# Kernel optimization log

Hardware: AMD Instinct MI355X
Metric: run time of the kernel (lower is better)

## Reference

```python
import jax, jax.numpy as jnp
import numpy as np

B, D, H = 32768, 256, 8
DH = D // H
SCALE = 1.0 / float(np.sqrt(DH))
# neighbor indices: for query node i, context = the other 3 nodes (in order)
NEIGH = np.array([[1, 2, 3], [0, 2, 3], [0, 1, 3], [0, 1, 2]], dtype=np.int32)


def setup_inputs() -> dict:
    key = jax.random.key(0)
    ks = jax.random.split(key, 6)
    s = 0.02
    mk = lambda k: jax.random.normal(k, (D, D), jnp.float32) * s
    return {
        "tokens": jax.random.normal(ks[0], (B, 4, D), jnp.float32),
        "Wq": mk(ks[1]),
        "Wk": mk(ks[2]),
        "Wv": mk(ks[3]),
        "Wr": mk(ks[4]),
        "Wo": mk(ks[5]),
        "ln_g": jnp.ones((D,), jnp.float32),
        "ln_b": jnp.zeros((D,), jnp.float32),
    }


def reference(tokens, Wq, Wk, Wv, Wr, Wo, ln_g, ln_b):
    # tokens: [B,4,D]. All 4 modality queries share one GCA block (share_gca=True),
    # so we batch the 4-node complete-graph message passing into one pass.
    neigh = jnp.asarray(NEIGH)
    ctx = tokens[:, neigh]                    # [B,4,3,D]
    Q = tokens @ Wq.T                         # [B,4,D]
    K = ctx @ Wk.T                            # [B,4,3,D]
    V = ctx @ Wv.T
    R = ctx @ Wr.T
    V_eff = jax.nn.sigmoid(R) * V             # gated values
    Qh = Q.reshape(B, 4, H, DH)
    Kh = K.reshape(B, 4, 3, H, DH)
    Vh = V_eff.reshape(B, 4, 3, H, DH)
    scores = jnp.einsum('bihd,bilhd->bihl', Qh, Kh) * SCALE   # [B,4,H,3]
    attn = jax.nn.softmax(scores, axis=-1)    # dropout = identity (eval mode)
    out = jnp.einsum('bihl,bilhd->bihd', attn, Vh).reshape(B, 4, D)
    out = out @ Wo.T
    y = tokens + out                          # residual
    mu = y.mean(-1, keepdims=True)
    var = y.var(-1, keepdims=True)
    y = (y - mu) / jnp.sqrt(var + 1e-5) * ln_g + ln_b   # LayerNorm
    # attn: [B,4,H,3] -> per-query attn maps (attn[:, i] == attn for modality-i query, [B,H,1,3] squeezed)
    return y, attn
```

## Files before the change

### kernel.cpp

```cpp
#include <hip/hip_runtime.h>
#include <stdint.h>


#define D_DIM   256
#define H_NUM   8
#define DH      32
#define RT      64
#define NTHR    1024
#define ROWS_TOT 131072
#define Y_SZ    33554432
#define SCALE_F 0.17677669529663687f
#define W_ELEMS 65536
#define WS_NEED (5 * W_ELEMS * 2)

#define SX_LD   264
#define SQK_LD  776
#define KOFF    256
#define VOFF    512
#define SY_LD   260

typedef __attribute__((ext_vector_type(8))) short bf16x8;
typedef __attribute__((ext_vector_type(4))) float f32x4;

__device__ __forceinline__ float b2f(uint16_t s) {
    union { uint32_t u; float f; } c; c.u = ((uint32_t)s) << 16; return c.f;
}
__device__ __forceinline__ uint16_t f2b(float f) {
    union { float f; uint32_t u; } c; c.f = f;
    return (uint16_t)((c.u + 0x7fffu + ((c.u >> 16) & 1u)) >> 16);
}
__device__ __forceinline__ bf16x8 cvt8(const float* p) {
    const float4 a = *(const float4*)p;
    const float4 b = *(const float4*)(p + 4);
    bf16x8 r;
    r[0] = (short)f2b(a.x); r[1] = (short)f2b(a.y);
    r[2] = (short)f2b(a.z); r[3] = (short)f2b(a.w);
    r[4] = (short)f2b(b.x); r[5] = (short)f2b(b.y);
    r[6] = (short)f2b(b.z); r[7] = (short)f2b(b.w);
    return r;
}

__global__ __launch_bounds__(256)
void conv_weights(const float* __restrict__ Wq, const float* __restrict__ Wk,
                  const float* __restrict__ Wv, const float* __restrict__ Wr,
                  const float* __restrict__ Wo, uint16_t* __restrict__ dst)
{
    const int m = blockIdx.x >> 6;
    const float* src = (m == 0) ? Wq : (m == 1) ? Wk : (m == 2) ? Wv
                     : (m == 3) ? Wr : Wo;
    const int base = (blockIdx.x & 63) * 1024 + threadIdx.x * 4;
    const float4 v = *(const float4*)&src[base];
    uint2 pk;
    pk.x = (uint32_t)f2b(v.x) | ((uint32_t)f2b(v.y) << 16);
    pk.y = (uint32_t)f2b(v.z) | ((uint32_t)f2b(v.w) << 16);
    *(uint2*)&dst[(size_t)m * W_ELEMS + base] = pk;
}

template<bool WBF16>
__global__ __launch_bounds__(NTHR, 4)
void cmaa_fused(const float* __restrict__ tok,
                const float* __restrict__ Wq, const float* __restrict__ Wk,
                const float* __restrict__ Wv, const float* __restrict__ Wr,
                const float* __restrict__ Wo,
                const uint16_t* __restrict__ wbf,
                const float* __restrict__ lng, const float* __restrict__ lnb,
                float* __restrict__ outp)
{
    __shared__ __align__(16) uint16_t sX [RT * SX_LD];
    __shared__ __align__(16) uint16_t sQK[RT * SQK_LD];

    const int tid  = threadIdx.x;
    const int wv   = tid >> 6;
    const int lane = tid & 63;
    const int l15  = lane & 15;
    const int quad = lane >> 4;
    const int R0   = blockIdx.x * RT;

    {
        const float* g = tok + (size_t)R0 * D_DIM;
        #pragma unroll
        for (int t = tid; t < RT * (D_DIM / 8); t += NTHR) {
            const int row = t >> 5, c = t & 31;
            *(bf16x8*)&sX[row * SX_LD + c * 8] = cvt8(&g[row * D_DIM + c * 8]);
        }
    }
    __syncthreads();

    {
        const int  colbase = (wv & 7) * 32;
        const bool qk = (wv < 8);
        const float*    WF0 = qk ? Wq : Wv;
        const float*    WF1 = qk ? Wk : Wr;
        const uint16_t* WB0 = wbf + (size_t)(qk ? 0 : 2) * W_ELEMS;
        const uint16_t* WB1 = WB0 + W_ELEMS;

        f32x4 acc[2][4][2];
        #pragma unroll
        for (int m = 0; m < 2; ++m)
            #pragma unroll
            for (int mt = 0; mt < 4; ++mt)
                #pragma unroll
                for (int nt = 0; nt < 2; ++nt)
                    acc[m][mt][nt] = (f32x4){0.f, 0.f, 0.f, 0.f};

        #pragma unroll
        for (int kk = 0; kk < 8; ++kk) {
            const int k0 = kk * 32;
            bf16x8 a[4];
            #pragma unroll
            for (int mt = 0; mt < 4; ++mt)
                a[mt] = *(const bf16x8*)&sX[(mt * 16 + l15) * SX_LD + k0 + quad * 8];

            bf16x8 b0[2], b1[2];
            #pragma unroll
            for (int nt = 0; nt < 2; ++nt) {
                const int wrow = colbase + nt * 16 + l15;
                if constexpr (WBF16) {
                    b0[nt] = *(const bf16x8*)&WB0[(size_t)wrow * D_DIM + k0 + quad * 8];
                    b1[nt] = *(const bf16x8*)&WB1[(size_t)wrow * D_DIM + k0 + quad * 8];
                } else {
                    b0[nt] = cvt8(&WF0[(size_t)wrow * D_DIM + k0 + quad * 8]);
                    b1[nt] = cvt8(&WF1[(size_t)wrow * D_DIM + k0 + quad * 8]);
                }
            }
            #pragma unroll
            for (int nt = 0; nt < 2; ++nt)
                #pragma unroll
                for (int mt = 0; mt < 4; ++mt)
                    acc[0][mt][nt] = __builtin_amdgcn_mfma_f32_16x16x32_bf16(a[mt], b0[nt], acc[0][mt][nt], 0, 0, 0);
            #pragma unroll
            for (int nt = 0; nt < 2; ++nt)
                #pragma unroll
                for (int mt = 0; mt < 4; ++mt)
                    acc[1][mt][nt] = __builtin_amdgcn_mfma_f32_16x16x32_bf16(a[mt], b1[nt], acc[1][mt][nt], 0, 0, 0);
        }

        if (qk) {
            #pragma unroll
            for (int mt = 0; mt < 4; ++mt)
                #pragma unroll
                for (int nt = 0; nt < 2; ++nt)
                    #pragma unroll
                    for (int r = 0; r < 4; ++r) {
                        const int row = mt * 16 + quad * 4 + r;
                        const int col = colbase + nt * 16 + l15;
                        sQK[row * SQK_LD + col]        = f2b(acc[0][mt][nt][r]);
                        sQK[row * SQK_LD + KOFF + col] = f2b(acc[1][mt][nt][r]);
                    }
        } else {
            #pragma unroll
            for (int mt = 0; mt < 4; ++mt)
                #pragma unroll
                for (int nt = 0; nt < 2; ++nt)
                    #pragma unroll
                    for (int r = 0; r < 4; ++r) {
                        const int row = mt * 16 + quad * 4 + r;
                        const int col = colbase + nt * 16 + l15;
                        const float vvv = acc[0][mt][nt][r];
                        const float rr  = acc[1][mt][nt][r];
                        const float sig = 1.f / (1.f + __expf(-rr));
                        sQK[row * SQK_LD + VOFF + col] = f2b(vvv * sig);
                    }
        }
    }
    __syncthreads();

    bf16x8 bw3[8];
    {
        const uint16_t* WoB = wbf + (size_t)4 * W_ELEMS;
        const int worow = wv * 16 + l15;
        #pragma unroll
        for (int kk = 0; kk < 8; ++kk) {
            if constexpr (WBF16)
                bw3[kk] = *(const bf16x8*)&WoB[(size_t)worow * D_DIM + kk * 32 + quad * 8];
            else
                bw3[kk] = cvt8(&Wo[(size_t)worow * D_DIM + kk * 32 + quad * 8]);
        }
    }

    {
        const int r    = tid >> 4;
        const int h    = (tid >> 1) & 7;
        const int half = tid & 1;
        const int gr = R0 + r;
        const int i  = r & 3;
        const int rb = r & ~3;
        int rn[3];
        #pragma unroll
        for (int l = 0; l < 3; ++l) { const int jj = l + (l >= i); rn[l] = rb + jj; }
        const int qoff = h * DH + half * 16;

        float q[16];
        #pragma unroll
        for (int t = 0; t < 2; ++t) {
            const bf16x8 v = *(const bf16x8*)&sQK[r * SQK_LD + qoff + t * 8];
            #pragma unroll
            for (int j = 0; j < 8; ++j) q[t * 8 + j] = b2f((uint16_t)v[j]);
        }

        float sc[3];
        #pragma unroll
        for (int l = 0; l < 3; ++l) {
            float s = 0.f;
            #pragma unroll
            for (int t = 0; t < 2; ++t) {
                const bf16x8 v = *(const bf16x8*)&sQK[rn[l] * SQK_LD + KOFF + qoff + t * 8];
                #pragma unroll
                for (int j = 0; j < 8; ++j) s += q[t * 8 + j] * b2f((uint16_t)v[j]);
            }
            s += __shfl_xor(s, 1);
            sc[l] = s * SCALE_F;
        }
        const float mx = fmaxf(sc[0], fmaxf(sc[1], sc[2]));
        const float e0 = __expf(sc[0] - mx), e1 = __expf(sc[1] - mx), e2 = __expf(sc[2] - mx);
        const float inv = 1.f / (e0 + e1 + e2);
        const float al[3] = { e0 * inv, e1 * inv, e2 * inv };

        if (half == 0) {
            float* ap = outp + Y_SZ + ((size_t)gr * H_NUM + h) * 3;
            ap[0] = al[0]; ap[1] = al[1]; ap[2] = al[2];
        }

        #pragma unroll
        for (int t = 0; t < 2; ++t) {
            float o[8] = {0.f,0.f,0.f,0.f,0.f,0.f,0.f,0.f};
            #pragma unroll
            for (int l = 0; l < 3; ++l) {
                const bf16x8 vv = *(const bf16x8*)&sQK[rn[l] * SQK_LD + VOFF + qoff + t * 8];
                #pragma unroll
                for (int j = 0; j < 8; ++j) o[j] += al[l] * b2f((uint16_t)vv[j]);
            }
            bf16x8 pk;
            #pragma unroll
            for (int j = 0; j < 8; ++j) pk[j] = (short)f2b(o[j]);
            *(bf16x8*)&sQK[r * SQK_LD + qoff + t * 8] = pk;
        }
    }
    __syncthreads();

    {
        f32x4 acc3[4];
        #pragma unroll
        for (int mt = 0; mt < 4; ++mt) acc3[mt] = (f32x4){0.f, 0.f, 0.f, 0.f};

        #pragma unroll
        for (int kk = 0; kk < 8; ++kk) {
            const int k0 = kk * 32;
            bf16x8 a[4];
            #pragma unroll
            for (int mt = 0; mt < 4; ++mt)
                a[mt] = *(const bf16x8*)&sQK[(mt * 16 + l15) * SQK_LD + k0 + quad * 8];
            #pragma unroll
            for (int mt = 0; mt < 4; ++mt)
                acc3[mt] = __builtin_amdgcn_mfma_f32_16x16x32_bf16(a[mt], bw3[kk], acc3[mt], 0, 0, 0);
        }
        __syncthreads();

        float* sY = (float*)sQK;
        #pragma unroll
        for (int mt = 0; mt < 4; ++mt)
            #pragma unroll
            for (int r = 0; r < 4; ++r) {
                const int row = mt * 16 + quad * 4 + r;
                const int col = wv * 16 + l15;
                sY[row * SY_LD + col] = acc3[mt][r] + b2f(sX[row * SX_LD + col]);
            }
    }
    __syncthreads();

    {
        const float* sY = (const float*)sQK;
        const int row = tid >> 4;
        const int sub = tid & 15;
        float vals[16];
        float s = 0.f;
        #pragma unroll
        for (int j = 0; j < 4; ++j) {
            const float4 v = *(const float4*)&sY[row * SY_LD + j * 64 + sub * 4];
            vals[j*4+0] = v.x; vals[j*4+1] = v.y; vals[j*4+2] = v.z; vals[j*4+3] = v.w;
            s += v.x + v.y + v.z + v.w;
        }
        s += __shfl_xor(s, 1); s += __shfl_xor(s, 2);
        s += __shfl_xor(s, 4); s += __shfl_xor(s, 8);
        const float mean = s * (1.f / 256.f);
        float s2 = 0.f;
        #pragma unroll
        for (int j = 0; j < 16; ++j) { const float d = vals[j] - mean; s2 += d * d; }
        s2 += __shfl_xor(s2, 1); s2 += __shfl_xor(s2, 2);
        s2 += __shfl_xor(s2, 4); s2 += __shfl_xor(s2, 8);
        const float var  = fmaxf(s2 * (1.f / 256.f), 0.f);
        const float rstd = rsqrtf(var + 1e-5f);

        float* orow = outp + (size_t)(R0 + row) * D_DIM;
        #pragma unroll
        for (int j = 0; j < 4; ++j) {
            const int col = j * 64 + sub * 4;
            const float4 g4 = *(const float4*)&lng[col];
            const float4 b4 = *(const float4*)&lnb[col];
            float4 o4;
            o4.x = (vals[j*4+0] - mean) * rstd * g4.x + b4.x;
            o4.y = (vals[j*4+1] - mean) * rstd * g4.y + b4.y;
            o4.z = (vals[j*4+2] - mean) * rstd * g4.z + b4.z;
            o4.w = (vals[j*4+3] - mean) * rstd * g4.w + b4.w;
            *(float4*)&orow[col] = o4;
        }
    }
}

extern "C" void kernel_launch(void* const* d_in, const int* in_sizes, int n_in,
                              void* d_out, int out_size, void* d_ws, size_t ws_size,
                              hipStream_t stream) {
    (void)in_sizes; (void)n_in; (void)out_size;
    const float* tok = (const float*)d_in[0];
    const float* Wq  = (const float*)d_in[1];
    const float* Wk  = (const float*)d_in[2];
    const float* Wv  = (const float*)d_in[3];
    const float* Wr  = (const float*)d_in[4];
    const float* Wo  = (const float*)d_in[5];
    const float* lng = (const float*)d_in[6];
    const float* lnb = (const float*)d_in[7];
    float* outp = (float*)d_out;
    uint16_t* wbf = (uint16_t*)d_ws;

    dim3 grid(ROWS_TOT / RT), block(NTHR);
    if (ws_size >= (size_t)WS_NEED) {
        conv_weights<<<dim3(320), dim3(256), 0, stream>>>(Wq, Wk, Wv, Wr, Wo, wbf);
        cmaa_fused<true><<<grid, block, 0, stream>>>(
            tok, Wq, Wk, Wv, Wr, Wo, wbf, lng, lnb, outp);
    } else {
        cmaa_fused<false><<<grid, block, 0, stream>>>(
            tok, Wq, Wk, Wv, Wr, Wo, wbf, lng, lnb, outp);
    }
}
```

Baseline: 432.8 us.

## Halve row tile to 32 with 512 threads and stagger weight/K access per block

```diff
diff --git a/kernel.cpp b/kernel.cpp
--- a/kernel.cpp
+++ b/kernel.cpp
@@ -5,8 +5,8 @@
 #define D_DIM   256
 #define H_NUM   8
 #define DH      32
-#define RT      64
-#define NTHR    1024
+#define RT      32
+#define NTHR    512
 #define ROWS_TOT 131072
 #define Y_SZ    33554432
 #define SCALE_F 0.17677669529663687f
@@ -75,6 +75,7 @@
     const int l15  = lane & 15;
     const int quad = lane >> 4;
     const int R0   = blockIdx.x * RT;
+    const int koff = blockIdx.x & 7;
 
     {
         const float* g = tok + (size_t)R0 * D_DIM;
@@ -87,33 +88,34 @@
     __syncthreads();
 
     {
-        const int  colbase = (wv & 7) * 32;
-        const bool qk = (wv < 8);
+        const int  colbase = (((wv & 3) + blockIdx.x) & 3) * 64;
+        const bool qk = (wv < 4);
         const float*    WF0 = qk ? Wq : Wv;
         const float*    WF1 = qk ? Wk : Wr;
         const uint16_t* WB0 = wbf + (size_t)(qk ? 0 : 2) * W_ELEMS;
         const uint16_t* WB1 = WB0 + W_ELEMS;
 
-        f32x4 acc[2][4][2];
+        f32x4 acc[2][2][4];
         #pragma unroll
         for (int m = 0; m < 2; ++m)
             #pragma unroll
-            for (int mt = 0; mt < 4; ++mt)
-                #pragma unroll
-                for (int nt = 0; nt < 2; ++nt)
+            for (int mt = 0; mt < 2; ++mt)
+                #pragma unroll
+                for (int nt = 0; nt < 4; ++nt)
                     acc[m][mt][nt] = (f32x4){0.f, 0.f, 0.f, 0.f};
 
         #pragma unroll
-        for (int kk = 0; kk < 8; ++kk) {
+        for (int i = 0; i < 8; ++i) {
+            const int kk = (i + koff) & 7;
             const int k0 = kk * 32;
-            bf16x8 a[4];
-            #pragma unroll
-            for (int mt = 0; mt < 4; ++mt)
+            bf16x8 a[2];
+            #pragma unroll
+            for (int mt = 0; mt < 2; ++mt)
                 a[mt] = *(const bf16x8*)&sX[(mt * 16 + l15) * SX_LD + k0 + quad * 8];
 
-            bf16x8 b0[2], b1[2];
-            #pragma unroll
-            for (int nt = 0; nt < 2; ++nt) {
+            bf16x8 b0[4], b1[4];
+            #pragma unroll
+            for (int nt = 0; nt < 4; ++nt) {
                 const int wrow = colbase + nt * 16 + l15;
                 if constexpr (WBF16) {
                     b0[nt] = *(const bf16x8*)&WB0[(size_t)wrow * D_DIM + k0 + quad * 8];
@@ -124,22 +126,22 @@
                 }
             }
             #pragma unroll
-            for (int nt = 0; nt < 2; ++nt)
-                #pragma unroll
-                for (int mt = 0; mt < 4; ++mt)
+            for (int nt = 0; nt < 4; ++nt)
+                #pragma unroll
+                for (int mt = 0; mt < 2; ++mt)
                     acc[0][mt][nt] = __builtin_amdgcn_mfma_f32_16x16x32_bf16(a[mt], b0[nt], acc[0][mt][nt], 0, 0, 0);
             #pragma unroll
-            for (int nt = 0; nt < 2; ++nt)
-                #pragma unroll
-                for (int mt = 0; mt < 4; ++mt)
+            for (int nt = 0; nt < 4; ++nt)
+                #pragma unroll
+                for (int mt = 0; mt < 2; ++mt)
                     acc[1][mt][nt] = __builtin_amdgcn_mfma_f32_16x16x32_bf16(a[mt], b1[nt], acc[1][mt][nt], 0, 0, 0);
         }
 
         if (qk) {
             #pragma unroll
-            for (int mt = 0; mt < 4; ++mt)
-                #pragma unroll
-                for (int nt = 0; nt < 2; ++nt)
+            for (int mt = 0; mt < 2; ++mt)
+                #pragma unroll
+                for (int nt = 0; nt < 4; ++nt)
                     #pragma unroll
                     for (int r = 0; r < 4; ++r) {
                         const int row = mt * 16 + quad * 4 + r;
@@ -149,9 +151,9 @@
                     }
         } else {
             #pragma unroll
-            for (int mt = 0; mt < 4; ++mt)
-                #pragma unroll
-                for (int nt = 0; nt < 2; ++nt)
+            for (int mt = 0; mt < 2; ++mt)
+                #pragma unroll
+                for (int nt = 0; nt < 4; ++nt)
                     #pragma unroll
                     for (int r = 0; r < 4; ++r) {
                         const int row = mt * 16 + quad * 4 + r;
@@ -165,16 +167,21 @@
     }
     __syncthreads();
 
-    bf16x8 bw3[8];
+    const int wob = ((wv + blockIdx.x) & 7) * 32;
+    bf16x8 bw3[2][8];
     {
         const uint16_t* WoB = wbf + (size_t)4 * W_ELEMS;
-        const int worow = wv * 16 + l15;
-        #pragma unroll
-        for (int kk = 0; kk < 8; ++kk) {
-            if constexpr (WBF16)
-                bw3[kk] = *(const bf16x8*)&WoB[(size_t)worow * D_DIM + kk * 32 + quad * 8];
-            else
-                bw3[kk] = cvt8(&Wo[(size_t)worow * D_DIM + kk * 32 + quad * 8]);
+        #pragma unroll
+        for (int nt = 0; nt < 2; ++nt) {
+            const int worow = wob + nt * 16 + l15;
+            #pragma unroll
+            for (int i = 0; i < 8; ++i) {
+                const int k0 = ((i + koff) & 7) * 32;
+                if constexpr (WBF16)
+                    bw3[nt][i] = *(const bf16x8*)&WoB[(size_t)worow * D_DIM + k0 + quad * 8];
+                else
+                    bw3[nt][i] = cvt8(&Wo[(size_t)worow * D_DIM + k0 + quad * 8]);
+            }
         }
     }
 
@@ -239,32 +246,39 @@
     __syncthreads();
 
     {
-        f32x4 acc3[4];
-        #pragma unroll
-        for (int mt = 0; mt < 4; ++mt) acc3[mt] = (f32x4){0.f, 0.f, 0.f, 0.f};
-
-        #pragma unroll
-        for (int kk = 0; kk < 8; ++kk) {
-            const int k0 = kk * 32;
-            bf16x8 a[4];
-            #pragma unroll
-            for (int mt = 0; mt < 4; ++mt)
+        f32x4 acc3[2][2];
+        #pragma unroll
+        for (int mt = 0; mt < 2; ++mt)
+            #pragma unroll
+            for (int nt = 0; nt < 2; ++nt)
+                acc3[mt][nt] = (f32x4){0.f, 0.f, 0.f, 0.f};
+
+        #pragma unroll
+        for (int i = 0; i < 8; ++i) {
+            const int k0 = ((i + koff) & 7) * 32;
+            bf16x8 a[2];
+            #pragma unroll
+            for (int mt = 0; mt < 2; ++mt)
                 a[mt] = *(const bf16x8*)&sQK[(mt * 16 + l15) * SQK_LD + k0 + quad * 8];
             #pragma unroll
-            for (int mt = 0; mt < 4; ++mt)
-                acc3[mt] = __builtin_amdgcn_mfma_f32_16x16x32_bf16(a[mt], bw3[kk], acc3[mt], 0, 0, 0);
+            for (int nt = 0; nt < 2; ++nt)
+                #pragma unroll
+                for (int mt = 0; mt < 2; ++mt)
+                    acc3[mt][nt] = __builtin_amdgcn_mfma_f32_16x16x32_bf16(a[mt], bw3[nt][i], acc3[mt][nt], 0, 0, 0);
         }
         __syncthreads();
 
         float* sY = (float*)sQK;
         #pragma unroll
-        for (int mt = 0; mt < 4; ++mt)
-            #pragma unroll
-            for (int r = 0; r < 4; ++r) {
-                const int row = mt * 16 + quad * 4 + r;
-                const int col = wv * 16 + l15;
-                sY[row * SY_LD + col] = acc3[mt][r] + b2f(sX[row * SX_LD + col]);
-            }
+        for (int mt = 0; mt < 2; ++mt)
+            #pragma unroll
+            for (int nt = 0; nt < 2; ++nt)
+                #pragma unroll
+                for (int r = 0; r < 4; ++r) {
+                    const int row = mt * 16 + quad * 4 + r;
+                    const int col = wob + nt * 16 + l15;
+                    sY[row * SY_LD + col] = acc3[mt][nt][r] + b2f(sX[row * SX_LD + col]);
+                }
     }
     __syncthreads();
 
```

Measured after the change: 511.6 us. 18.2% more time.
